# Optimization experiments

Measured on AMD Instinct MI355X. Metric: run time of the kernel, lower is better.

The kernel has to match this reference:

```python
import jax, jax.numpy as jnp
import numpy as np

N, E, B, D, L = 50000, 1600000, 128, 64, 5
BN_EPS = 1e-5

def _bn(x, g, b, m, v):
    # eval-mode BatchNorm1d with running stats
    return (x - m) * jax.lax.rsqrt(v + BN_EPS) * g + b

def setup_inputs() -> dict:
    key = jax.random.key(0)
    ks = iter(jax.random.split(key, 64))
    w = 1.0 / np.sqrt(D)
    def nrm(shape, s):
        return jax.random.normal(next(ks), shape, jnp.float32) * s
    def var(shape):
        return jax.random.uniform(next(ks), shape, jnp.float32) + 0.5
    inp = {
        "x": nrm((N, D), 1.0),
        "lin_W": nrm((D, D), w), "lin_b": nrm((D,), w),
        "eps": jnp.zeros((L,), jnp.float32),
        "gin_W1": nrm((L, D, D), w), "gin_b1": nrm((L, D), w),
        "gin_bn_g": jnp.ones((L, D), jnp.float32), "gin_bn_b": jnp.zeros((L, D), jnp.float32),
        "gin_bn_m": nrm((L, D), 0.1), "gin_bn_v": var((L, D)),
        "gin_W2": nrm((L, D, D), w), "gin_b2": nrm((L, D), w),
        "bn_g": jnp.ones((L, D), jnp.float32), "bn_b": jnp.zeros((L, D), jnp.float32),
        "bn_m": nrm((L, D), 0.1), "bn_v": var((L, D)),
        "vn_emb": jnp.zeros((D,), jnp.float32),  # init constant 0 per source
        "vn_W1": nrm((L - 1, D, D), w), "vn_b1": nrm((L - 1, D), w),
        "vn_bn1_g": jnp.ones((L - 1, D), jnp.float32), "vn_bn1_b": jnp.zeros((L - 1, D), jnp.float32),
        "vn_bn1_m": nrm((L - 1, D), 0.1), "vn_bn1_v": var((L - 1, D)),
        "vn_W2": nrm((L - 1, D, D), w), "vn_b2": nrm((L - 1, D), w),
        "vn_bn2_g": jnp.ones((L - 1, D), jnp.float32), "vn_bn2_b": jnp.zeros((L - 1, D), jnp.float32),
        "vn_bn2_m": nrm((L - 1, D), 0.1), "vn_bn2_v": var((L - 1, D)),
        "src": jax.random.randint(next(ks), (E,), 0, N, jnp.int32),
        "dst": jax.random.randint(next(ks), (E,), 0, N, jnp.int32),
        "batch_id": jnp.sort(jax.random.randint(next(ks), (N,), 0, B, jnp.int32)),
    }
    return inp

def reference(x, lin_W, lin_b, eps, gin_W1, gin_b1, gin_bn_g, gin_bn_b, gin_bn_m, gin_bn_v,
              gin_W2, gin_b2, bn_g, bn_b, bn_m, bn_v, vn_emb,
              vn_W1, vn_b1, vn_bn1_g, vn_bn1_b, vn_bn1_m, vn_bn1_v,
              vn_W2, vn_b2, vn_bn2_g, vn_bn2_b, vn_bn2_m, vn_bn2_v,
              src, dst, batch_id):
    n = x.shape[0]
    h = x @ lin_W + lin_b                       # input linear [N, D]
    h_list = [h]
    vn = jnp.broadcast_to(vn_emb, (B, D))       # per-graph virtual node [B, D]
    for l in range(L):
        h_list[l] = h_list[l] + vn[batch_id]    # virtual-node broadcast to nodes
        hl = h_list[l]
        # GINConv: sum over incoming edges of relu(src feature)
        agg = jax.ops.segment_sum(jax.nn.relu(hl[src]), dst, num_segments=n)
        z = (1.0 + eps[l]) * hl + agg
        z = z @ gin_W1[l] + gin_b1[l]
        z = jax.nn.relu(_bn(z, gin_bn_g[l], gin_bn_b[l], gin_bn_m[l], gin_bn_v[l]))
        z = z @ gin_W2[l] + gin_b2[l]
        z = _bn(z, bn_g[l], bn_b[l], bn_m[l], bn_v[l])  # outer batchnorm
        if l != L - 1:
            z = jax.nn.relu(z)                  # dropout is identity in eval mode
        h_list.append(z)
        if l < L - 1:
            # sum-pool nodes per graph, update virtual node via MLP
            vt = jax.ops.segment_sum(hl, batch_id, num_segments=B) + vn
            vt = vt @ vn_W1[l] + vn_b1[l]
            vt = jax.nn.relu(_bn(vt, vn_bn1_g[l], vn_bn1_b[l], vn_bn1_m[l], vn_bn1_v[l]))
            vt = vt @ vn_W2[l] + vn_b2[l]
            vn = jax.nn.relu(_bn(vt, vn_bn2_g[l], vn_bn2_b[l], vn_bn2_m[l], vn_bn2_v[l]))
    # JK='sum' in the source sums h_list[0..num_layers-1] (excludes final entry)
    out = h_list[0]
    for l in range(1, L):
        out = out + h_list[l]
    return out
```

## Files before the change

kernel.cpp:

```cpp
#include <hip/hip_runtime.h>

#define N_NODES 50000
#define N_EDGES 1600000
#define NB 128
#define GB 782
#define CAP 80
#define NODE_RANGE 6250
#define EDGE_BLOCKS 6250
#define INIT_BLOCKS 32

__device__ __forceinline__ unsigned short f2bf(float f) {
    unsigned u = __float_as_uint(f);
    unsigned r = (u + 0x7FFFu + ((u >> 16) & 1u)) >> 16;
    return (unsigned short)r;
}
__device__ __forceinline__ float bflo(unsigned u) { return __uint_as_float(u << 16); }
__device__ __forceinline__ float bfhi(unsigned u) { return __uint_as_float(u & 0xFFFF0000u); }

__global__ __launch_bounds__(256) void k_build(
    const int* __restrict__ src, const int* __restrict__ dst,
    int* __restrict__ cnt, unsigned short* __restrict__ csr_src,
    const float* __restrict__ vn_emb, float* __restrict__ pooled) {
    int bid = blockIdx.x;
    if (bid >= EDGE_BLOCKS * 8) {
        int t = (bid - EDGE_BLOCKS * 8) * 256 + threadIdx.x;
        pooled[t] = vn_emb[t & 63];
        return;
    }
    int range = bid & 7;
    int e = (bid >> 3) * 256 + threadIdx.x;
    int d = dst[e];
    if (d / NODE_RANGE != range) return;
    int pos = atomicAdd(&cnt[d], 1);
    if (pos < CAP) csr_src[(size_t)d * CAP + pos] = (unsigned short)src[e];
}

__global__ __launch_bounds__(256) void k_lin_pre(
    const float* __restrict__ in, const float* __restrict__ W,
    const float* __restrict__ bias, const float* __restrict__ vn_emb,
    const int* __restrict__ batch_id,
    float* __restrict__ h, float* __restrict__ out,
    unsigned short* __restrict__ rbuf, float* __restrict__ pooled) {
    __shared__ float sW[64 * 64];
    __shared__ float sIn[64 * 68];
    int tid = threadIdx.x;
    int row0 = blockIdx.x * 64;

    const float4* W4 = (const float4*)W;
#pragma unroll
    for (int i = 0; i < 4; ++i) ((float4*)sW)[tid + 256 * i] = W4[tid + 256 * i];
    const float4* in4 = (const float4*)in;
#pragma unroll
    for (int i = 0; i < 4; ++i) {
        int idx = tid + 256 * i;
        int r = idx >> 4, j = idx & 15;
        float4 val = make_float4(0.f, 0.f, 0.f, 0.f);
        if (row0 + r < N_NODES) val = in4[(size_t)(row0 + r) * 16 + j];
        ((float4*)(sIn + r * 68))[j] = val;
    }
    __syncthreads();

    int c4 = (tid & 15) * 4;
    int rl = (tid >> 4) * 4;
    float acc[4][4] = {{0.f}};
#pragma unroll 8
    for (int k = 0; k < 64; ++k) {
        float4 wv = *(const float4*)(sW + k * 64 + c4);
        float a0 = sIn[(rl + 0) * 68 + k];
        float a1 = sIn[(rl + 1) * 68 + k];
        float a2 = sIn[(rl + 2) * 68 + k];
        float a3 = sIn[(rl + 3) * 68 + k];
        acc[0][0] += a0 * wv.x; acc[0][1] += a0 * wv.y; acc[0][2] += a0 * wv.z; acc[0][3] += a0 * wv.w;
        acc[1][0] += a1 * wv.x; acc[1][1] += a1 * wv.y; acc[1][2] += a1 * wv.z; acc[1][3] += a1 * wv.w;
        acc[2][0] += a2 * wv.x; acc[2][1] += a2 * wv.y; acc[2][2] += a2 * wv.z; acc[2][3] += a2 * wv.w;
        acc[3][0] += a3 * wv.x; acc[3][1] += a3 * wv.y; acc[3][2] += a3 * wv.z; acc[3][3] += a3 * wv.w;
    }
    float shf[4];
#pragma unroll
    for (int j = 0; j < 4; ++j) shf[j] = bias[c4 + j] + vn_emb[c4 + j];

    int lane = tid & 63;
    int wave = tid >> 6;
    int wr0 = row0 + wave * 16;
    bool full = (wr0 + 15 < N_NODES);
    bool fast = full && (batch_id[wr0] == batch_id[wr0 + 15]);
    float4 pacc = make_float4(0.f, 0.f, 0.f, 0.f);
#pragma unroll
    for (int r = 0; r < 4; ++r) {
        int row = row0 + rl + r;
        if (row >= N_NODES) continue;
        float4 v;
        v.x = acc[r][0] + shf[0];
        v.y = acc[r][1] + shf[1];
        v.z = acc[r][2] + shf[2];
        v.w = acc[r][3] + shf[3];
        *(float4*)(h + (size_t)row * 64 + c4) = v;
        *(float4*)(out + (size_t)row * 64 + c4) = v;
        ushort4 rb;
        rb.x = f2bf(fmaxf(v.x, 0.f)); rb.y = f2bf(fmaxf(v.y, 0.f));
        rb.z = f2bf(fmaxf(v.z, 0.f)); rb.w = f2bf(fmaxf(v.w, 0.f));
        *(ushort4*)(rbuf + (size_t)row * 64 + c4) = rb;
        if (fast) {
            pacc.x += v.x; pacc.y += v.y; pacc.z += v.z; pacc.w += v.w;
        } else {
            int b = batch_id[row];
            atomicAdd(&pooled[b * 64 + c4 + 0], v.x);
            atomicAdd(&pooled[b * 64 + c4 + 1], v.y);
            atomicAdd(&pooled[b * 64 + c4 + 2], v.z);
            atomicAdd(&pooled[b * 64 + c4 + 3], v.w);
        }
    }
    if (fast) {
        pacc.x += __shfl_xor(pacc.x, 16); pacc.x += __shfl_xor(pacc.x, 32);
        pacc.y += __shfl_xor(pacc.y, 16); pacc.y += __shfl_xor(pacc.y, 32);
        pacc.z += __shfl_xor(pacc.z, 16); pacc.z += __shfl_xor(pacc.z, 32);
        pacc.w += __shfl_xor(pacc.w, 16); pacc.w += __shfl_xor(pacc.w, 32);
        if ((lane >> 4) == 0) {
            int b = batch_id[wr0];
            atomicAdd(&pooled[b * 64 + c4 + 0], pacc.x);
            atomicAdd(&pooled[b * 64 + c4 + 1], pacc.y);
            atomicAdd(&pooled[b * 64 + c4 + 2], pacc.z);
            atomicAdd(&pooled[b * 64 + c4 + 3], pacc.w);
        }
    }
}

__global__ __launch_bounds__(512) void k_gin(
    const float* __restrict__ h_in, const float* __restrict__ eps, int l,
    const int* __restrict__ cnt, const unsigned short* __restrict__ csr_src,
    const unsigned short* __restrict__ rbuf_in,
    const float* __restrict__ W1, const float* __restrict__ b1,
    const float* __restrict__ g1, const float* __restrict__ be1,
    const float* __restrict__ m1, const float* __restrict__ v1,
    const float* __restrict__ W2, const float* __restrict__ b2,
    const float* __restrict__ g2, const float* __restrict__ be2,
    const float* __restrict__ m2, const float* __restrict__ v2,
    const float* __restrict__ vn, const int* __restrict__ batch_id,
    float* __restrict__ h, float* __restrict__ out,
    unsigned short* __restrict__ rbuf_out, float* __restrict__ pooled,
    int last) {
    __shared__ float sW[64 * 64];
    __shared__ float sIn[64 * 68];
    int tid = threadIdx.x;
    int row0 = blockIdx.x * 64;
    int lane = tid & 63;
    int wave = tid >> 6;

#pragma unroll
    for (int i = 0; i < 2; ++i)
        ((float4*)sW)[tid + 512 * i] = ((const float4*)W1)[tid + 512 * i];

    {
        int g = lane >> 3, f4 = lane & 7;
        int row = row0 + wave * 8 + g;
        float e1 = 1.0f + eps[l];
        const uint4* tab4 = (const uint4*)rbuf_in;
        float aL0 = 0.f, aH0 = 0.f, aL1 = 0.f, aH1 = 0.f;
        float aL2 = 0.f, aH2 = 0.f, aL3 = 0.f, aH3 = 0.f;
        if (row < N_NODES) {
            int deg = cnt[row]; if (deg > CAP) deg = CAP;
            const unsigned short* rowp = csr_src + (size_t)row * CAP;
            int e = 0;
            for (; e + 7 < deg; e += 8) {
                ushort4 sa = *(const ushort4*)(rowp + e);
                ushort4 sb = *(const ushort4*)(rowp + e + 4);
                uint4 u0 = tab4[(size_t)sa.x * 8 + f4];
                uint4 u1 = tab4[(size_t)sa.y * 8 + f4];
                uint4 u2 = tab4[(size_t)sa.z * 8 + f4];
                uint4 u3 = tab4[(size_t)sa.w * 8 + f4];
                uint4 u4 = tab4[(size_t)sb.x * 8 + f4];
                uint4 u5 = tab4[(size_t)sb.y * 8 + f4];
                uint4 u6 = tab4[(size_t)sb.z * 8 + f4];
                uint4 u7 = tab4[(size_t)sb.w * 8 + f4];
                aL0 += bflo(u0.x); aH0 += bfhi(u0.x); aL1 += bflo(u0.y); aH1 += bfhi(u0.y);
                aL2 += bflo(u0.z); aH2 += bfhi(u0.z); aL3 += bflo(u0.w); aH3 += bfhi(u0.w);
                aL0 += bflo(u1.x); aH0 += bfhi(u1.x); aL1 += bflo(u1.y); aH1 += bfhi(u1.y);
                aL2 += bflo(u1.z); aH2 += bfhi(u1.z); aL3 += bflo(u1.w); aH3 += bfhi(u1.w);
                aL0 += bflo(u2.x); aH0 += bfhi(u2.x); aL1 += bflo(u2.y); aH1 += bfhi(u2.y);
                aL2 += bflo(u2.z); aH2 += bfhi(u2.z); aL3 += bflo(u2.w); aH3 += bfhi(u2.w);
                aL0 += bflo(u3.x); aH0 += bfhi(u3.x); aL1 += bflo(u3.y); aH1 += bfhi(u3.y);
                aL2 += bflo(u3.z); aH2 += bfhi(u3.z); aL3 += bflo(u3.w); aH3 += bfhi(u3.w);
                aL0 += bflo(u4.x); aH0 += bfhi(u4.x); aL1 += bflo(u4.y); aH1 += bfhi(u4.y);
                aL2 += bflo(u4.z); aH2 += bfhi(u4.z); aL3 += bflo(u4.w); aH3 += bfhi(u4.w);
                aL0 += bflo(u5.x); aH0 += bfhi(u5.x); aL1 += bflo(u5.y); aH1 += bfhi(u5.y);
                aL2 += bflo(u5.z); aH2 += bfhi(u5.z); aL3 += bflo(u5.w); aH3 += bfhi(u5.w);
                aL0 += bflo(u6.x); aH0 += bfhi(u6.x); aL1 += bflo(u6.y); aH1 += bfhi(u6.y);
                aL2 += bflo(u6.z); aH2 += bfhi(u6.z); aL3 += bflo(u6.w); aH3 += bfhi(u6.w);
                aL0 += bflo(u7.x); aH0 += bfhi(u7.x); aL1 += bflo(u7.y); aH1 += bfhi(u7.y);
                aL2 += bflo(u7.z); aH2 += bfhi(u7.z); aL3 += bflo(u7.w); aH3 += bfhi(u7.w);
            }
            for (; e + 3 < deg; e += 4) {
                ushort4 sa = *(const ushort4*)(rowp + e);
                uint4 u0 = tab4[(size_t)sa.x * 8 + f4];
                uint4 u1 = tab4[(size_t)sa.y * 8 + f4];
                uint4 u2 = tab4[(size_t)sa.z * 8 + f4];
                uint4 u3 = tab4[(size_t)sa.w * 8 + f4];
                aL0 += bflo(u0.x); aH0 += bfhi(u0.x); aL1 += bflo(u0.y); aH1 += bfhi(u0.y);
                aL2 += bflo(u0.z); aH2 += bfhi(u0.z); aL3 += bflo(u0.w); aH3 += bfhi(u0.w);
                aL0 += bflo(u1.x); aH0 += bfhi(u1.x); aL1 += bflo(u1.y); aH1 += bfhi(u1.y);
                aL2 += bflo(u1.z); aH2 += bfhi(u1.z); aL3 += bflo(u1.w); aH3 += bfhi(u1.w);
                aL0 += bflo(u2.x); aH0 += bfhi(u2.x); aL1 += bflo(u2.y); aH1 += bfhi(u2.y);
                aL2 += bflo(u2.z); aH2 += bfhi(u2.z); aL3 += bflo(u2.w); aH3 += bfhi(u2.w);
                aL0 += bflo(u3.x); aH0 += bfhi(u3.x); aL1 += bflo(u3.y); aH1 += bfhi(u3.y);
                aL2 += bflo(u3.z); aH2 += bfhi(u3.z); aL3 += bflo(u3.w); aH3 += bfhi(u3.w);
            }
            for (; e < deg; ++e) {
                uint4 u = tab4[(size_t)rowp[e] * 8 + f4];
                aL0 += bflo(u.x); aH0 += bfhi(u.x); aL1 += bflo(u.y); aH1 += bfhi(u.y);
                aL2 += bflo(u.z); aH2 += bfhi(u.z); aL3 += bflo(u.w); aH3 += bfhi(u.w);
            }
        }
        float* sp = sIn + (wave * 8 + g) * 68 + f4 * 8;
        if (row < N_NODES) {
            const float* hp = h_in + (size_t)row * 64 + f4 * 8;
            float4 h0 = *(const float4*)hp;
            float4 h1 = *(const float4*)(hp + 4);
            float4 o0, o1;
            o0.x = e1 * h0.x + aL0; o0.y = e1 * h0.y + aH0;
            o0.z = e1 * h0.z + aL1; o0.w = e1 * h0.w + aH1;
            o1.x = e1 * h1.x + aL2; o1.y = e1 * h1.y + aH2;
            o1.z = e1 * h1.z + aL3; o1.w = e1 * h1.w + aH3;
            *(float4*)sp = o0;
            *(float4*)(sp + 4) = o1;
        } else {
            *(float4*)sp = make_float4(0.f, 0.f, 0.f, 0.f);
            *(float4*)(sp + 4) = make_float4(0.f, 0.f, 0.f, 0.f);
        }
    }
    __syncthreads();

    int c4 = (tid & 15) * 4;
    int rg = tid >> 4;
    float acc[2][4] = {{0.f}};
#pragma unroll 8
    for (int k = 0; k < 64; ++k) {
        float4 wv = *(const float4*)(sW + k * 64 + c4);
        float a0 = sIn[(2 * rg + 0) * 68 + k];
        float a1 = sIn[(2 * rg + 1) * 68 + k];
        acc[0][0] += a0 * wv.x; acc[0][1] += a0 * wv.y; acc[0][2] += a0 * wv.z; acc[0][3] += a0 * wv.w;
        acc[1][0] += a1 * wv.x; acc[1][1] += a1 * wv.y; acc[1][2] += a1 * wv.z; acc[1][3] += a1 * wv.w;
    }
    float scl[4], shf[4];
#pragma unroll
    for (int j = 0; j < 4; ++j) {
        int c = c4 + j;
        float sc = g1[c] * rsqrtf(v1[c] + 1e-5f);
        scl[j] = sc;
        shf[j] = be1[c] - m1[c] * sc + b1[c] * sc;
    }
    __syncthreads();
#pragma unroll
    for (int i = 0; i < 2; ++i) {
        float4 z;
        z.x = fmaxf(acc[i][0] * scl[0] + shf[0], 0.f);
        z.y = fmaxf(acc[i][1] * scl[1] + shf[1], 0.f);
        z.z = fmaxf(acc[i][2] * scl[2] + shf[2], 0.f);
        z.w = fmaxf(acc[i][3] * scl[3] + shf[3], 0.f);
        *(float4*)(sIn + (2 * rg + i) * 68 + c4) = z;
    }
#pragma unroll
    for (int i = 0; i < 2; ++i)
        ((float4*)sW)[tid + 512 * i] = ((const float4*)W2)[tid + 512 * i];
    __syncthreads();

    float acc2[2][4] = {{0.f}};
#pragma unroll 8
    for (int k = 0; k < 64; ++k) {
        float4 wv = *(const float4*)(sW + k * 64 + c4);
        float a0 = sIn[(2 * rg + 0) * 68 + k];
        float a1 = sIn[(2 * rg + 1) * 68 + k];
        acc2[0][0] += a0 * wv.x; acc2[0][1] += a0 * wv.y; acc2[0][2] += a0 * wv.z; acc2[0][3] += a0 * wv.w;
        acc2[1][0] += a1 * wv.x; acc2[1][1] += a1 * wv.y; acc2[1][2] += a1 * wv.z; acc2[1][3] += a1 * wv.w;
    }
#pragma unroll
    for (int j = 0; j < 4; ++j) {
        int c = c4 + j;
        float sc = g2[c] * rsqrtf(v2[c] + 1e-5f);
        scl[j] = sc;
        shf[j] = be2[c] - m2[c] * sc + b2[c] * sc;
    }

    int wr0 = row0 + wave * 8;
    bool full = (wr0 + 7 < N_NODES);
    bool fast = (!last) && full && (batch_id[wr0] == batch_id[wr0 + 7]);
    float4 pacc = make_float4(0.f, 0.f, 0.f, 0.f);
#pragma unroll
    for (int r = 0; r < 2; ++r) {
        int row = row0 + rg * 2 + r;
        if (row >= N_NODES) continue;
        int b = batch_id[row];
        float4 vv = *(const float4*)(vn + b * 64 + c4);
        float4 v;
        v.x = fmaxf(acc2[r][0] * scl[0] + shf[0], 0.f) + vv.x;
        v.y = fmaxf(acc2[r][1] * scl[1] + shf[1], 0.f) + vv.y;
        v.z = fmaxf(acc2[r][2] * scl[2] + shf[2], 0.f) + vv.z;
        v.w = fmaxf(acc2[r][3] * scl[3] + shf[3], 0.f) + vv.w;
        float4 o = *(const float4*)(out + (size_t)row * 64 + c4);
        o.x += v.x; o.y += v.y; o.z += v.z; o.w += v.w;
        *(float4*)(out + (size_t)row * 64 + c4) = o;
        if (!last) {
            *(float4*)(h + (size_t)row * 64 + c4) = v;
            ushort4 rb;
            rb.x = f2bf(fmaxf(v.x, 0.f)); rb.y = f2bf(fmaxf(v.y, 0.f));
            rb.z = f2bf(fmaxf(v.z, 0.f)); rb.w = f2bf(fmaxf(v.w, 0.f));
            *(ushort4*)(rbuf_out + (size_t)row * 64 + c4) = rb;
            if (fast) {
                pacc.x += v.x; pacc.y += v.y; pacc.z += v.z; pacc.w += v.w;
            } else {
                atomicAdd(&pooled[b * 64 + c4 + 0], v.x);
                atomicAdd(&pooled[b * 64 + c4 + 1], v.y);
                atomicAdd(&pooled[b * 64 + c4 + 2], v.z);
                atomicAdd(&pooled[b * 64 + c4 + 3], v.w);
            }
        }
    }
    if (fast) {
        pacc.x += __shfl_xor(pacc.x, 16); pacc.x += __shfl_xor(pacc.x, 32);
        pacc.y += __shfl_xor(pacc.y, 16); pacc.y += __shfl_xor(pacc.y, 32);
        pacc.z += __shfl_xor(pacc.z, 16); pacc.z += __shfl_xor(pacc.z, 32);
        pacc.w += __shfl_xor(pacc.w, 16); pacc.w += __shfl_xor(pacc.w, 32);
        if ((lane >> 4) == 0) {
            int b = batch_id[wr0];
            atomicAdd(&pooled[b * 64 + c4 + 0], pacc.x);
            atomicAdd(&pooled[b * 64 + c4 + 1], pacc.y);
            atomicAdd(&pooled[b * 64 + c4 + 2], pacc.z);
            atomicAdd(&pooled[b * 64 + c4 + 3], pacc.w);
        }
    }
}

__global__ __launch_bounds__(1024) void k_vnmlp(
    const float* __restrict__ pooled_in,
    const float* __restrict__ W1, const float* __restrict__ b1,
    const float* __restrict__ g1, const float* __restrict__ be1,
    const float* __restrict__ m1, const float* __restrict__ v1,
    const float* __restrict__ W2, const float* __restrict__ b2,
    const float* __restrict__ g2, const float* __restrict__ be2,
    const float* __restrict__ m2, const float* __restrict__ v2,
    float* __restrict__ vn_out, float* __restrict__ pooled_out) {
    __shared__ float sP[128 * 68];
    __shared__ float sW[64 * 64];
    int tid = threadIdx.x;

    ((float4*)sW)[tid] = ((const float4*)W1)[tid];
#pragma unroll
    for (int i = 0; i < 2; ++i) {
        int idx = tid + 1024 * i;
        int r = idx >> 4, j = idx & 15;
        ((float4*)(sP + r * 68))[j] = ((const float4*)pooled_in)[idx];
    }
    __syncthreads();

    int c4 = (tid & 15) * 4, rg = tid >> 4;
    float acc[2][4] = {{0.f}};
#pragma unroll 8
    for (int k = 0; k < 64; ++k) {
        float4 w = *(const float4*)(sW + k * 64 + c4);
#pragma unroll
        for (int i = 0; i < 2; ++i) {
            float a = sP[(rg * 2 + i) * 68 + k];
            acc[i][0] += a * w.x; acc[i][1] += a * w.y;
            acc[i][2] += a * w.z; acc[i][3] += a * w.w;
        }
    }
    float scl[4], shf[4];
#pragma unroll
    for (int j = 0; j < 4; ++j) {
        int c = c4 + j;
        float sc = g1[c] * rsqrtf(v1[c] + 1e-5f);
        scl[j] = sc;
        shf[j] = be1[c] - m1[c] * sc + b1[c] * sc;
    }
    __syncthreads();
#pragma unroll
    for (int i = 0; i < 2; ++i) {
        float4 z;
        z.x = fmaxf(acc[i][0] * scl[0] + shf[0], 0.f);
        z.y = fmaxf(acc[i][1] * scl[1] + shf[1], 0.f);
        z.z = fmaxf(acc[i][2] * scl[2] + shf[2], 0.f);
        z.w = fmaxf(acc[i][3] * scl[3] + shf[3], 0.f);
        *(float4*)(sP + (rg * 2 + i) * 68 + c4) = z;
    }
    ((float4*)sW)[tid] = ((const float4*)W2)[tid];
    __syncthreads();

    float acc2[2][4] = {{0.f}};
#pragma unroll 8
    for (int k = 0; k < 64; ++k) {
        float4 w = *(const float4*)(sW + k * 64 + c4);
#pragma unroll
        for (int i = 0; i < 2; ++i) {
            float a = sP[(rg * 2 + i) * 68 + k];
            acc2[i][0] += a * w.x; acc2[i][1] += a * w.y;
            acc2[i][2] += a * w.z; acc2[i][3] += a * w.w;
        }
    }
#pragma unroll
    for (int j = 0; j < 4; ++j) {
        int c = c4 + j;
        float sc = g2[c] * rsqrtf(v2[c] + 1e-5f);
        scl[j] = sc;
        shf[j] = be2[c] - m2[c] * sc + b2[c] * sc;
    }
#pragma unroll
    for (int i = 0; i < 2; ++i) {
        int row = rg * 2 + i;
        float4 o;
        o.x = fmaxf(acc2[i][0] * scl[0] + shf[0], 0.f);
        o.y = fmaxf(acc2[i][1] * scl[1] + shf[1], 0.f);
        o.z = fmaxf(acc2[i][2] * scl[2] + shf[2], 0.f);
        o.w = fmaxf(acc2[i][3] * scl[3] + shf[3], 0.f);
        *(float4*)(vn_out + row * 64 + c4) = o;
        *(float4*)(pooled_out + row * 64 + c4) = o;
    }
}

extern "C" void kernel_launch(void* const* d_in, const int* in_sizes, int n_in,
                              void* d_out, int out_size, void* d_ws, size_t ws_size,
                              hipStream_t stream) {
    const float* x      = (const float*)d_in[0];
    const float* lin_W  = (const float*)d_in[1];
    const float* lin_b  = (const float*)d_in[2];
    const float* eps    = (const float*)d_in[3];
    const float* gin_W1 = (const float*)d_in[4];
    const float* gin_b1 = (const float*)d_in[5];
    const float* gbn_g  = (const float*)d_in[6];
    const float* gbn_b  = (const float*)d_in[7];
    const float* gbn_m  = (const float*)d_in[8];
    const float* gbn_v  = (const float*)d_in[9];
    const float* gin_W2 = (const float*)d_in[10];
    const float* gin_b2 = (const float*)d_in[11];
    const float* bn_g   = (const float*)d_in[12];
    const float* bn_b   = (const float*)d_in[13];
    const float* bn_m   = (const float*)d_in[14];
    const float* bn_v   = (const float*)d_in[15];
    const float* vn_emb = (const float*)d_in[16];
    const float* vn_W1  = (const float*)d_in[17];
    const float* vn_b1  = (const float*)d_in[18];
    const float* v1g    = (const float*)d_in[19];
    const float* v1b    = (const float*)d_in[20];
    const float* v1m    = (const float*)d_in[21];
    const float* v1v    = (const float*)d_in[22];
    const float* vn_W2  = (const float*)d_in[23];
    const float* vn_b2  = (const float*)d_in[24];
    const float* v2g    = (const float*)d_in[25];
    const float* v2b    = (const float*)d_in[26];
    const float* v2m    = (const float*)d_in[27];
    const float* v2v    = (const float*)d_in[28];
    const int* src      = (const int*)d_in[29];
    const int* dst      = (const int*)d_in[30];
    const int* batch_id = (const int*)d_in[31];
    float* out = (float*)d_out;

    float* h      = (float*)d_ws;
    unsigned short* rbufA = (unsigned short*)(h + (size_t)N_NODES * 64);
    unsigned short* rbufB = rbufA + (size_t)N_NODES * 64;
    float* vn     = (float*)(rbufB + (size_t)N_NODES * 64);
    float* pooled = vn  + (size_t)NB * 64;
    int*   cnt    = (int*)(pooled + (size_t)NB * 64);
    unsigned short* csr_src = (unsigned short*)(cnt + N_NODES);

    hipMemsetAsync(cnt, 0, N_NODES * sizeof(int), stream);
    k_build<<<EDGE_BLOCKS * 8 + INIT_BLOCKS, 256, 0, stream>>>(src, dst, cnt, csr_src,
                                                               vn_emb, pooled);

    k_lin_pre<<<GB, 256, 0, stream>>>(x, lin_W, lin_b, vn_emb, batch_id,
                                      h, out, rbufA, pooled);

    for (int l = 0; l < 4; ++l) {
        unsigned short* rin  = (l & 1) ? rbufB : rbufA;
        unsigned short* rout = (l & 1) ? rbufA : rbufB;
        k_vnmlp<<<1, 1024, 0, stream>>>(pooled,
                                        vn_W1 + l * 4096, vn_b1 + l * 64,
                                        v1g + l * 64, v1b + l * 64, v1m + l * 64, v1v + l * 64,
                                        vn_W2 + l * 4096, vn_b2 + l * 64,
                                        v2g + l * 64, v2b + l * 64, v2m + l * 64, v2v + l * 64,
                                        vn, pooled);
        k_gin<<<GB, 512, 0, stream>>>(h, eps, l, cnt, csr_src, rin,
                                      gin_W1 + l * 4096, gin_b1 + l * 64,
                                      gbn_g + l * 64, gbn_b + l * 64,
                                      gbn_m + l * 64, gbn_v + l * 64,
                                      gin_W2 + l * 4096, gin_b2 + l * 64,
                                      bn_g + l * 64, bn_b + l * 64,
                                      bn_m + l * 64, bn_v + l * 64,
                                      vn, batch_id, h, out, rout, pooled,
                                      l == 3);
    }
}
```

Before: 469.2 us.

## Fuse virtual-node MLP into GIN kernel, computing per-block vn redundantly

Removes the separate single-block k_vnmlp launch per layer. Each GIN block now recomputes the virtual-node MLP for the few graphs its 64 rows cover and keeps the results in LDS. Pooled sums and vn states move to per-layer buffers, zeroed once by an enlarged memset, so no cross-block ordering hazard arises. This trades four serial tiny launches for redundant MLP work in every block, with W1/W2 read from global memory per block.

```diff
diff --git a/kernel.cpp b/kernel.cpp
--- a/kernel.cpp
+++ b/kernel.cpp
@@ -8,6 +8,7 @@
 #define NODE_RANGE 6250
 #define EDGE_BLOCKS 6250
 #define INIT_BLOCKS 32
+#define VNSZ (NB * 64)
 
 __device__ __forceinline__ unsigned short f2bf(float f) {
     unsigned u = __float_as_uint(f);
@@ -20,11 +21,11 @@
 __global__ __launch_bounds__(256) void k_build(
     const int* __restrict__ src, const int* __restrict__ dst,
     int* __restrict__ cnt, unsigned short* __restrict__ csr_src,
-    const float* __restrict__ vn_emb, float* __restrict__ pooled) {
+    const float* __restrict__ vn_emb, float* __restrict__ vnbuf0) {
     int bid = blockIdx.x;
     if (bid >= EDGE_BLOCKS * 8) {
         int t = (bid - EDGE_BLOCKS * 8) * 256 + threadIdx.x;
-        pooled[t] = vn_emb[t & 63];
+        vnbuf0[t] = vn_emb[t & 63];
         return;
     }
     int range = bid & 7;
@@ -135,16 +136,65 @@
     const float* __restrict__ W2, const float* __restrict__ b2,
     const float* __restrict__ g2, const float* __restrict__ be2,
     const float* __restrict__ m2, const float* __restrict__ v2,
-    const float* __restrict__ vn, const int* __restrict__ batch_id,
+    const float* __restrict__ vW1, const float* __restrict__ vb1,
+    const float* __restrict__ vg1, const float* __restrict__ vbe1,
+    const float* __restrict__ vm1, const float* __restrict__ vv1,
+    const float* __restrict__ vW2, const float* __restrict__ vb2,
+    const float* __restrict__ vg2, const float* __restrict__ vbe2,
+    const float* __restrict__ vm2, const float* __restrict__ vv2,
+    const float* __restrict__ pooledRawL, const float* __restrict__ vnprev,
+    float* __restrict__ vnnext, const int* __restrict__ batch_id,
     float* __restrict__ h, float* __restrict__ out,
-    unsigned short* __restrict__ rbuf_out, float* __restrict__ pooled,
+    unsigned short* __restrict__ rbuf_out, float* __restrict__ pooledNext,
     int last) {
     __shared__ float sW[64 * 64];
     __shared__ float sIn[64 * 68];
+    __shared__ float vnLDS[16][64];
+    __shared__ float zT[8][64];
     int tid = threadIdx.x;
     int row0 = blockIdx.x * 64;
     int lane = tid & 63;
     int wave = tid >> 6;
+
+    int row_hi = row0 + 63; if (row_hi >= N_NODES) row_hi = N_NODES - 1;
+    int b_lo = batch_id[row0];
+    {
+        int nb = batch_id[row_hi] - b_lo + 1;
+        if (nb > 16) nb = 16;
+        int c = lane;
+        float sc1 = vg1[c] * rsqrtf(vv1[c] + 1e-5f);
+        float sh1 = vbe1[c] - vm1[c] * sc1 + vb1[c] * sc1;
+        float sc2 = vg2[c] * rsqrtf(vv2[c] + 1e-5f);
+        float sh2 = vbe2[c] - vm2[c] * sc2 + vb2[c] * sc2;
+        int nTrips = (nb + 7) & ~7;
+        for (int gi = wave; gi < nTrips; gi += 8) {
+            bool act = gi < nb;
+            int b = b_lo + (act ? gi : 0);
+            const float* pr = pooledRawL + b * 64;
+            const float* vp = vnprev + b * 64;
+            float s1 = 0.f;
+            for (int k = 0; k < 64; k += 4) {
+                float4 p4 = *(const float4*)(pr + k);
+                float4 q4 = *(const float4*)(vp + k);
+                p4.x += q4.x; p4.y += q4.y; p4.z += q4.z; p4.w += q4.w;
+                s1 += p4.x * vW1[(k + 0) * 64 + c] + p4.y * vW1[(k + 1) * 64 + c]
+                    + p4.z * vW1[(k + 2) * 64 + c] + p4.w * vW1[(k + 3) * 64 + c];
+            }
+            zT[wave][c] = fmaxf(sc1 * s1 + sh1, 0.f);
+            float s2 = 0.f;
+            for (int k = 0; k < 64; k += 4) {
+                s2 += zT[wave][k + 0] * vW2[(k + 0) * 64 + c]
+                    + zT[wave][k + 1] * vW2[(k + 1) * 64 + c]
+                    + zT[wave][k + 2] * vW2[(k + 2) * 64 + c]
+                    + zT[wave][k + 3] * vW2[(k + 3) * 64 + c];
+            }
+            float vr = fmaxf(sc2 * s2 + sh2, 0.f);
+            if (act) {
+                vnLDS[gi][c] = vr;
+                if (!last) vnnext[b * 64 + c] = vr;
+            }
+        }
+    }
 
 #pragma unroll
     for (int i = 0; i < 2; ++i)
@@ -289,7 +339,8 @@
         int row = row0 + rg * 2 + r;
         if (row >= N_NODES) continue;
         int b = batch_id[row];
-        float4 vv = *(const float4*)(vn + b * 64 + c4);
+        int idx = b - b_lo; if (idx > 15) idx = 15;
+        float4 vv = *(const float4*)(&vnLDS[idx][c4]);
         float4 v;
         v.x = fmaxf(acc2[r][0] * scl[0] + shf[0], 0.f) + vv.x;
         v.y = fmaxf(acc2[r][1] * scl[1] + shf[1], 0.f) + vv.y;
@@ -307,10 +358,10 @@
             if (fast) {
                 pacc.x += v.x; pacc.y += v.y; pacc.z += v.z; pacc.w += v.w;
             } else {
-                atomicAdd(&pooled[b * 64 + c4 + 0], v.x);
-                atomicAdd(&pooled[b * 64 + c4 + 1], v.y);
-                atomicAdd(&pooled[b * 64 + c4 + 2], v.z);
-                atomicAdd(&pooled[b * 64 + c4 + 3], v.w);
+                atomicAdd(&pooledNext[b * 64 + c4 + 0], v.x);
+                atomicAdd(&pooledNext[b * 64 + c4 + 1], v.y);
+                atomicAdd(&pooledNext[b * 64 + c4 + 2], v.z);
+                atomicAdd(&pooledNext[b * 64 + c4 + 3], v.w);
             }
         }
     }
@@ -321,97 +372,11 @@
         pacc.w += __shfl_xor(pacc.w, 16); pacc.w += __shfl_xor(pacc.w, 32);
         if ((lane >> 4) == 0) {
             int b = batch_id[wr0];
-            atomicAdd(&pooled[b * 64 + c4 + 0], pacc.x);
-            atomicAdd(&pooled[b * 64 + c4 + 1], pacc.y);
-            atomicAdd(&pooled[b * 64 + c4 + 2], pacc.z);
-            atomicAdd(&pooled[b * 64 + c4 + 3], pacc.w);
-        }
-    }
-}
-
-__global__ __launch_bounds__(1024) void k_vnmlp(
-    const float* __restrict__ pooled_in,
-    const float* __restrict__ W1, const float* __restrict__ b1,
-    const float* __restrict__ g1, const float* __restrict__ be1,
-    const float* __restrict__ m1, const float* __restrict__ v1,
-    const float* __restrict__ W2, const float* __restrict__ b2,
-    const float* __restrict__ g2, const float* __restrict__ be2,
-    const float* __restrict__ m2, const float* __restrict__ v2,
-    float* __restrict__ vn_out, float* __restrict__ pooled_out) {
-    __shared__ float sP[128 * 68];
-    __shared__ float sW[64 * 64];
-    int tid = threadIdx.x;
-
-    ((float4*)sW)[tid] = ((const float4*)W1)[tid];
-#pragma unroll
-    for (int i = 0; i < 2; ++i) {
-        int idx = tid + 1024 * i;
-        int r = idx >> 4, j = idx & 15;
-        ((float4*)(sP + r * 68))[j] = ((const float4*)pooled_in)[idx];
-    }
-    __syncthreads();
-
-    int c4 = (tid & 15) * 4, rg = tid >> 4;
-    float acc[2][4] = {{0.f}};
-#pragma unroll 8
-    for (int k = 0; k < 64; ++k) {
-        float4 w = *(const float4*)(sW + k * 64 + c4);
-#pragma unroll
-        for (int i = 0; i < 2; ++i) {
-            float a = sP[(rg * 2 + i) * 68 + k];
-            acc[i][0] += a * w.x; acc[i][1] += a * w.y;
-            acc[i][2] += a * w.z; acc[i][3] += a * w.w;
-        }
-    }
-    float scl[4], shf[4];
-#pragma unroll
-    for (int j = 0; j < 4; ++j) {
-        int c = c4 + j;
-        float sc = g1[c] * rsqrtf(v1[c] + 1e-5f);
-        scl[j] = sc;
-        shf[j] = be1[c] - m1[c] * sc + b1[c] * sc;
-    }
-    __syncthreads();
-#pragma unroll
-    for (int i = 0; i < 2; ++i) {
-        float4 z;
-        z.x = fmaxf(acc[i][0] * scl[0] + shf[0], 0.f);
-        z.y = fmaxf(acc[i][1] * scl[1] + shf[1], 0.f);
-        z.z = fmaxf(acc[i][2] * scl[2] + shf[2], 0.f);
-        z.w = fmaxf(acc[i][3] * scl[3] + shf[3], 0.f);
-        *(float4*)(sP + (rg * 2 + i) * 68 + c4) = z;
-    }
-    ((float4*)sW)[tid] = ((const float4*)W2)[tid];
-    __syncthreads();
-
-    float acc2[2][4] = {{0.f}};
-#pragma unroll 8
-    for (int k = 0; k < 64; ++k) {
-        float4 w = *(const float4*)(sW + k * 64 + c4);
-#pragma unroll
-        for (int i = 0; i < 2; ++i) {
-            float a = sP[(rg * 2 + i) * 68 + k];
-            acc2[i][0] += a * w.x; acc2[i][1] += a * w.y;
-            acc2[i][2] += a * w.z; acc2[i][3] += a * w.w;
-        }
-    }
-#pragma unroll
-    for (int j = 0; j < 4; ++j) {
-        int c = c4 + j;
-        float sc = g2[c] * rsqrtf(v2[c] + 1e-5f);
-        scl[j] = sc;
-        shf[j] = be2[c] - m2[c] * sc + b2[c] * sc;
-    }
-#pragma unroll
-    for (int i = 0; i < 2; ++i) {
-        int row = rg * 2 + i;
-        float4 o;
-        o.x = fmaxf(acc2[i][0] * scl[0] + shf[0], 0.f);
-        o.y = fmaxf(acc2[i][1] * scl[1] + shf[1], 0.f);
-        o.z = fmaxf(acc2[i][2] * scl[2] + shf[2], 0.f);
-        o.w = fmaxf(acc2[i][3] * scl[3] + shf[3], 0.f);
-        *(float4*)(vn_out + row * 64 + c4) = o;
-        *(float4*)(pooled_out + row * 64 + c4) = o;
+            atomicAdd(&pooledNext[b * 64 + c4 + 0], pacc.x);
+            atomicAdd(&pooledNext[b * 64 + c4 + 1], pacc.y);
+            atomicAdd(&pooledNext[b * 64 + c4 + 2], pacc.z);
+            atomicAdd(&pooledNext[b * 64 + c4 + 3], pacc.w);
+        }
     }
 }
 
@@ -455,27 +420,22 @@
     float* h      = (float*)d_ws;
     unsigned short* rbufA = (unsigned short*)(h + (size_t)N_NODES * 64);
     unsigned short* rbufB = rbufA + (size_t)N_NODES * 64;
-    float* vn     = (float*)(rbufB + (size_t)N_NODES * 64);
-    float* pooled = vn  + (size_t)NB * 64;
-    int*   cnt    = (int*)(pooled + (size_t)NB * 64);
-    unsigned short* csr_src = (unsigned short*)(cnt + N_NODES);
-
-    hipMemsetAsync(cnt, 0, N_NODES * sizeof(int), stream);
+    float* vnbuf  = (float*)(rbufB + (size_t)N_NODES * 64);
+    int*   cnt    = (int*)(vnbuf + 4 * VNSZ);
+    float* pooledRaw = (float*)(cnt + N_NODES);
+    unsigned short* csr_src = (unsigned short*)(pooledRaw + 4 * VNSZ);
+
+    hipMemsetAsync(cnt, 0, N_NODES * sizeof(int) + 4 * VNSZ * sizeof(float), stream);
     k_build<<<EDGE_BLOCKS * 8 + INIT_BLOCKS, 256, 0, stream>>>(src, dst, cnt, csr_src,
-                                                               vn_emb, pooled);
+                                                               vn_emb, vnbuf);
 
     k_lin_pre<<<GB, 256, 0, stream>>>(x, lin_W, lin_b, vn_emb, batch_id,
-                                      h, out, rbufA, pooled);
+                                      h, out, rbufA, pooledRaw);
 
     for (int l = 0; l < 4; ++l) {
         unsigned short* rin  = (l & 1) ? rbufB : rbufA;
         unsigned short* rout = (l & 1) ? rbufA : rbufB;
-        k_vnmlp<<<1, 1024, 0, stream>>>(pooled,
-                                        vn_W1 + l * 4096, vn_b1 + l * 64,
-                                        v1g + l * 64, v1b + l * 64, v1m + l * 64, v1v + l * 64,
-                                        vn_W2 + l * 4096, vn_b2 + l * 64,
-                                        v2g + l * 64, v2b + l * 64, v2m + l * 64, v2v + l * 64,
-                                        vn, pooled);
+        int last = (l == 3);
         k_gin<<<GB, 512, 0, stream>>>(h, eps, l, cnt, csr_src, rin,
                                       gin_W1 + l * 4096, gin_b1 + l * 64,
                                       gbn_g + l * 64, gbn_b + l * 64,
@@ -483,7 +443,15 @@
                                       gin_W2 + l * 4096, gin_b2 + l * 64,
                                       bn_g + l * 64, bn_b + l * 64,
                                       bn_m + l * 64, bn_v + l * 64,
-                                      vn, batch_id, h, out, rout, pooled,
-                                      l == 3);
+                                      vn_W1 + l * 4096, vn_b1 + l * 64,
+                                      v1g + l * 64, v1b + l * 64, v1m + l * 64, v1v + l * 64,
+                                      vn_W2 + l * 4096, vn_b2 + l * 64,
+                                      v2g + l * 64, v2b + l * 64, v2m + l * 64, v2v + l * 64,
+                                      pooledRaw + l * VNSZ,
+                                      vnbuf + l * VNSZ,
+                                      last ? vnbuf : vnbuf + (l + 1) * VNSZ,
+                                      batch_id, h, out, rout,
+                                      last ? pooledRaw : pooledRaw + (l + 1) * VNSZ,
+                                      last);
     }
 }
```

Result: slower. 490.8 us (+4.6%).
